# Performance work log

Hardware: AMD Instinct MI355X
Metric: run time of the kernel (lower is better)

The kernel has to match this reference:

```python
import jax, jax.numpy as jnp
import numpy as np

B, S, W = 128, 256, 1
DEPTH = 655            # MathTypeKeysMax
UNITS = 128
PROBLEM_BUCKETS = 32


def setup_inputs() -> dict:
    key = jax.random.key(0)
    ks = jax.random.split(key, 14)
    ri = lambda k, shape, hi: jax.random.randint(k, shape, 0, hi, dtype=jnp.int32)
    K = 4 * DEPTH * W  # flattened per-timestep feature width = 2620
    return {
        'move_count': ri(ks[0], (B,), 100),
        'moves_remaining': ri(ks[1], (B,), 100),
        'last_rule': ri(ks[2], (B,), 12),
        'node_count': ri(ks[3], (B,), 64),
        'problem_type': ri(ks[4], (B,), PROBLEM_BUCKETS),
        'bwd_vectors': ri(ks[5], (B, S, W), DEPTH),
        'fwd_vectors': ri(ks[6], (B, S, W), DEPTH),
        'last_bwd_vectors': ri(ks[7], (B, S, W), DEPTH),
        'last_fwd_vectors': ri(ks[8], (B, S, W), DEPTH),
        'W_dense': jax.random.normal(ks[9], (K, UNITS), jnp.float32) * (1.0 / np.sqrt(K)),
        'b_dense': jnp.zeros((UNITS,), jnp.float32),
        'Wx': jax.random.normal(ks[10], (UNITS, 4 * UNITS), jnp.float32) * (1.0 / np.sqrt(UNITS)),
        'Wh': jax.random.normal(ks[11], (UNITS, 4 * UNITS), jnp.float32) * (1.0 / np.sqrt(UNITS)),
        'b_lstm': jnp.zeros((4 * UNITS,), jnp.float32),
    }


def _lstm(x, Wx, Wh, b):
    # x: [B, S, U] -> (seq hidden [B, S, U], final hidden [B, U]); keras gate order i,f,c,o
    U = Wh.shape[0]
    bsz = x.shape[0]
    # precompute input projections once: [S, B, 4U]
    xz = jnp.einsum('bsu,uv->sbv', x, Wx) + b

    def step(carry, zt):
        h, c = carry
        z = zt + h @ Wh
        i, f, g, o = jnp.split(z, 4, axis=-1)
        i = jax.nn.sigmoid(i)
        f = jax.nn.sigmoid(f)
        g = jnp.tanh(g)
        o = jax.nn.sigmoid(o)
        c = f * c + i * g
        h = o * jnp.tanh(c)
        return (h, c), h

    init = (jnp.zeros((bsz, U), x.dtype), jnp.zeros((bsz, U), x.dtype))
    (h_last, _), hs = jax.lax.scan(step, init, xz)
    return jnp.transpose(hs, (1, 0, 2)), h_last


def reference(move_count, moves_remaining, last_rule, node_count, problem_type,
              bwd_vectors, fwd_vectors, last_bwd_vectors, last_fwd_vectors,
              W_dense, b_dense, Wx, Wh, b_lstm):
    f32 = lambda a: a.astype(jnp.float32)
    # DenseFeatures context extraction: 3 numeric int columns + 32-bucket indicator
    context_inputs = jnp.concatenate([
        f32(last_rule)[:, None],
        f32(move_count)[:, None],
        f32(node_count)[:, None],
        jax.nn.one_hot(problem_type, PROBLEM_BUCKETS, dtype=jnp.float32),
    ], axis=-1)  # [B, 35]

    sequence_length = bwd_vectors.shape[1]
    # one-hot each [B,S,W] sequence to [B,S,W,DEPTH], concat on last axis -> [B,S,W,4*DEPTH]
    oh = jnp.concatenate([
        jax.nn.one_hot(bwd_vectors, DEPTH, dtype=jnp.float32),
        jax.nn.one_hot(fwd_vectors, DEPTH, dtype=jnp.float32),
        jax.nn.one_hot(last_bwd_vectors, DEPTH, dtype=jnp.float32),
        jax.nn.one_hot(last_fwd_vectors, DEPTH, dtype=jnp.float32),
    ], axis=-1)
    bsz = oh.shape[0]
    # per-example Flatten keeps leading S dim, so the loop == one batched matmul
    flat = oh.reshape(bsz, sequence_length, -1)      # [B, S, 4*DEPTH*W]
    outputs = jnp.einsum('bsk,ku->bsu', flat, W_dense) + b_dense  # [B, S, U]

    hidden_states, lstm_vectors = _lstm(outputs, Wx, Wh, b_lstm)
    return (context_inputs, lstm_vectors, hidden_states, sequence_length)
```

## Files before the change

kernel.cpp:

```cpp
#include <hip/hip_runtime.h>
#include <cstdint>

#define BB   128
#define SS   256
#define NDEPTH 655
#define UU   128
#define VV   512
#define NPB  32

#define STEP_BARRIER()                                          \
    do {                                                        \
        asm volatile("s_waitcnt lgkmcnt(0)" ::: "memory");      \
        __builtin_amdgcn_s_barrier();                           \
        __builtin_amdgcn_sched_barrier(0);                      \
    } while (0)

__global__ void context_kernel(const int* __restrict__ last_rule,
                               const int* __restrict__ move_count,
                               const int* __restrict__ node_count,
                               const int* __restrict__ problem_type,
                               float* __restrict__ out, int write_seq) {
    int i = blockIdx.x * blockDim.x + threadIdx.x;
    if (i < BB * 35) {
        int b = i / 35, c = i % 35;
        float v;
        if (c == 0)      v = (float)last_rule[b];
        else if (c == 1) v = (float)move_count[b];
        else if (c == 2) v = (float)node_count[b];
        else             v = (problem_type[b] == (c - 3)) ? 1.0f : 0.0f;
        out[i] = v;
    }
    if (write_seq && i == 0)
        out[(size_t)BB*35 + (size_t)BB*UU + (size_t)BB*SS*UU] = (float)SS;
}

__global__ void wdwx_kernel(const float* __restrict__ Wd,
                            const float* __restrict__ Wx,
                            const float* __restrict__ b_dense,
                            const float* __restrict__ b_lstm,
                            float* __restrict__ WdWx,
                            float* __restrict__ base) {
    int v  = threadIdx.x;
    int k0 = blockIdx.x * 4;
    const float* wd0 = Wd + (size_t)k0 * UU;
    float a0 = 0.f, a1 = 0.f, a2 = 0.f, a3 = 0.f;
    for (int u = 0; u < UU; ++u) {
        float wx = Wx[u * VV + v];
        a0 = fmaf(wd0[u],        wx, a0);
        a1 = fmaf(wd0[UU + u],   wx, a1);
        a2 = fmaf(wd0[2*UU + u], wx, a2);
        a3 = fmaf(wd0[3*UU + u], wx, a3);
    }
    WdWx[(size_t)(k0+0)*VV + v] = a0;
    WdWx[(size_t)(k0+1)*VV + v] = a1;
    WdWx[(size_t)(k0+2)*VV + v] = a2;
    WdWx[(size_t)(k0+3)*VV + v] = a3;
    if (blockIdx.x == 0) {
        float a = 0.f;
        for (int u = 0; u < UU; ++u) a = fmaf(b_dense[u], Wx[u * VV + v], a);
        base[v] = a + b_lstm[v];
    }
}

__global__ __launch_bounds__(512, 2)
void lstm_kernel(const int* __restrict__ bwd,  const int* __restrict__ fwd,
                 const int* __restrict__ lbwd, const int* __restrict__ lfwd,
                 const float* __restrict__ WdWx,
                 const float* __restrict__ base,
                 const float* __restrict__ Wh,
                 float* __restrict__ hidden_states,
                 float* __restrict__ lstm_vectors) {
    const int b    = blockIdx.x;
    const int t    = threadIdx.x;
    const int lane = t & 63;
    const int w    = t >> 6;
    const int q    = lane & 3;
    const int u    = w * 16 + (lane >> 2);
    const int col  = q * UU + u;

    __shared__ __align__(16) float h_buf[2][144];
    __shared__ int idx_lds[SS][4];

    float wh[128];
    #pragma unroll
    for (int kk = 0; kk < 32; ++kk) {
        #pragma unroll
        for (int g = 0; g < 4; ++g)
            wh[kk*4+g] = Wh[(size_t)(32*q + kk) * VV + g*UU + u];
    }

    for (int s = t; s < SS; s += 512) {
        idx_lds[s][0] =            bwd [b*SS + s];
        idx_lds[s][1] =   NDEPTH + fwd [b*SS + s];
        idx_lds[s][2] = 2*NDEPTH + lbwd[b*SS + s];
        idx_lds[s][3] = 3*NDEPTH + lfwd[b*SS + s];
    }
    if (t < UU) h_buf[0][36*(t>>5) + (t&31)] = 0.0f;
    float c    = 0.0f;
    float bias = base[col];
    __syncthreads();

    float g0 = WdWx[(size_t)idx_lds[0][0] * VV + col];
    float g1 = WdWx[(size_t)idx_lds[0][1] * VV + col];
    float g2 = WdWx[(size_t)idx_lds[0][2] * VV + col];
    float g3 = WdWx[(size_t)idx_lds[0][3] * VV + col];

    const bool b0 = (q & 1) != 0;
    const bool b1 = (q & 2) != 0;

    int p = 0;
    for (int s = 0; s < SS; ++s) {
        float z = bias + (g0 + g1) + (g2 + g3);
        if (s + 1 < SS) {
            g0 = WdWx[(size_t)idx_lds[s+1][0] * VV + col];
            g1 = WdWx[(size_t)idx_lds[s+1][1] * VV + col];
            g2 = WdWx[(size_t)idx_lds[s+1][2] * VV + col];
            g3 = WdWx[(size_t)idx_lds[s+1][3] * VV + col];
        }

        const float* hb = h_buf[p] + 36 * q;
        float pp0 = 0.f, pp1 = 0.f, pp2 = 0.f, pp3 = 0.f;
        #pragma unroll
        for (int kk = 0; kk < 32; kk += 4) {
            float4 hv = *(const float4*)(hb + kk);
            pp0 = fmaf(hv.x, wh[(kk+0)*4+0], pp0);
            pp1 = fmaf(hv.x, wh[(kk+0)*4+1], pp1);
            pp2 = fmaf(hv.x, wh[(kk+0)*4+2], pp2);
            pp3 = fmaf(hv.x, wh[(kk+0)*4+3], pp3);
            pp0 = fmaf(hv.y, wh[(kk+1)*4+0], pp0);
            pp1 = fmaf(hv.y, wh[(kk+1)*4+1], pp1);
            pp2 = fmaf(hv.y, wh[(kk+1)*4+2], pp2);
            pp3 = fmaf(hv.y, wh[(kk+1)*4+3], pp3);
            pp0 = fmaf(hv.z, wh[(kk+2)*4+0], pp0);
            pp1 = fmaf(hv.z, wh[(kk+2)*4+1], pp1);
            pp2 = fmaf(hv.z, wh[(kk+2)*4+2], pp2);
            pp3 = fmaf(hv.z, wh[(kk+2)*4+3], pp3);
            pp0 = fmaf(hv.w, wh[(kk+3)*4+0], pp0);
            pp1 = fmaf(hv.w, wh[(kk+3)*4+1], pp1);
            pp2 = fmaf(hv.w, wh[(kk+3)*4+2], pp2);
            pp3 = fmaf(hv.w, wh[(kk+3)*4+3], pp3);
        }

        float keepA = b0 ? pp1 : pp0;
        float keepB = b0 ? pp3 : pp2;
        float sendA = b0 ? pp0 : pp1;
        float sendB = b0 ? pp2 : pp3;
        float sA = keepA + __shfl_xor(sendA, 1);
        float sB = keepB + __shfl_xor(sendB, 1);
        float send2 = b1 ? sA : sB;
        z += (b1 ? sB : sA) + __shfl_xor(send2, 2);

        float xs = (q == 2) ? 2.0f * z : z;
        float sg = __fdividef(1.0f, 1.0f + __expf(-xs));
        float a  = (q == 2) ? 2.0f * sg - 1.0f : sg;

        float v1 = __shfl_xor(a, 1);
        float v2 = __shfl_xor(a, 2);
        float v3 = __shfl_xor(v1, 2);
        float ig = (q & 1) ? v1 * v3 : a * v2;
        float gf = (q & 1) ? ((q & 2) ? v2 : a)
                           : ((q & 2) ? v3 : v1);
        float go = (q & 1) ? ((q & 2) ? a  : v2)
                           : ((q & 2) ? v1 : v3);
        c = fmaf(gf, c, ig);
        float e  = __expf(2.0f * c);
        float tc = 1.0f - __fdividef(2.0f, e + 1.0f);
        float h  = go * tc;

        if (q == 0) {
            h_buf[p ^ 1][36*(u>>5) + (u&31)] = h;
            hidden_states[((size_t)b * SS + s) * UU + u] = h;
        }
        STEP_BARRIER();
        p ^= 1;
    }
    if (t < UU) lstm_vectors[(size_t)b * UU + t] = h_buf[p][36*(t>>5) + (t&31)];
}

extern "C" void kernel_launch(void* const* d_in, const int* in_sizes, int n_in,
                              void* d_out, int out_size, void* d_ws, size_t ws_size,
                              hipStream_t stream) {
    const int* move_count   = (const int*)d_in[0];
    const int* last_rule    = (const int*)d_in[2];
    const int* node_count   = (const int*)d_in[3];
    const int* problem_type = (const int*)d_in[4];
    const int* bwd          = (const int*)d_in[5];
    const int* fwd          = (const int*)d_in[6];
    const int* lbwd         = (const int*)d_in[7];
    const int* lfwd         = (const int*)d_in[8];
    const float* Wd         = (const float*)d_in[9];
    const float* b_dense    = (const float*)d_in[10];
    const float* Wx         = (const float*)d_in[11];
    const float* Wh         = (const float*)d_in[12];
    const float* b_lstm     = (const float*)d_in[13];

    float* out  = (float*)d_out;
    float* WdWx = (float*)d_ws;
    float* base = WdWx + (size_t)(4 * NDEPTH) * VV;

    float* lstm_out = out + BB * 35;
    float* hs_out   = lstm_out + BB * UU;
    int write_seq = (out_size > BB*35 + BB*UU + BB*SS*UU) ? 1 : 0;

    context_kernel<<<(BB*35 + 255)/256, 256, 0, stream>>>(
        last_rule, move_count, node_count, problem_type, out, write_seq);
    wdwx_kernel<<<NDEPTH, VV, 0, stream>>>(Wd, Wx, b_dense, b_lstm, WdWx, base);
    lstm_kernel<<<BB, 512, 0, stream>>>(bwd, fwd, lbwd, lfwd, WdWx, base, Wh,
                                        hs_out, lstm_out);
}
```

Before: 316.9 us.

## Use fp16 dot2 for recurrent matvec, fuse context into WdWx kernel

The recurrent h·Wh product now keeps Wh and h in packed fp16 and uses the fdot2 instruction, halving LDS reads and FMA count per step on the serial critical path. The context kernel is folded into the WdWx precompute kernel, which now computes 20 rows per block over 131 blocks, removing one launch. The final hidden state is kept in a register instead of being reread from shared memory. Rounding h and Wh to fp16 adds error that accumulates over 256 recurrent steps.

```diff
diff --git a/kernel.cpp b/kernel.cpp
--- a/kernel.cpp
+++ b/kernel.cpp
@@ -7,6 +7,18 @@
 #define UU   128
 #define VV   512
 #define NPB  32
+#define ROWS_PER_BLK 20
+
+typedef _Float16 f16;
+typedef _Float16 f16x2 __attribute__((ext_vector_type(2)));
+
+#if __has_builtin(__builtin_amdgcn_fdot2)
+#define FDOT2(a, b, c) __builtin_amdgcn_fdot2((a), (b), (c), false)
+#else
+static __device__ __forceinline__ float FDOT2(f16x2 a, f16x2 b, float c) {
+    return c + (float)a.x * (float)b.x + (float)a.y * (float)b.y;
+}
+#endif
 
 #define STEP_BARRIER()                                          \
     do {                                                        \
@@ -15,49 +27,47 @@
         __builtin_amdgcn_sched_barrier(0);                      \
     } while (0)
 
-__global__ void context_kernel(const int* __restrict__ last_rule,
-                               const int* __restrict__ move_count,
-                               const int* __restrict__ node_count,
-                               const int* __restrict__ problem_type,
-                               float* __restrict__ out, int write_seq) {
-    int i = blockIdx.x * blockDim.x + threadIdx.x;
-    if (i < BB * 35) {
-        int b = i / 35, c = i % 35;
-        float v;
-        if (c == 0)      v = (float)last_rule[b];
-        else if (c == 1) v = (float)move_count[b];
-        else if (c == 2) v = (float)node_count[b];
-        else             v = (problem_type[b] == (c - 3)) ? 1.0f : 0.0f;
-        out[i] = v;
-    }
-    if (write_seq && i == 0)
-        out[(size_t)BB*35 + (size_t)BB*UU + (size_t)BB*SS*UU] = (float)SS;
-}
-
 __global__ void wdwx_kernel(const float* __restrict__ Wd,
                             const float* __restrict__ Wx,
                             const float* __restrict__ b_dense,
                             const float* __restrict__ b_lstm,
+                            const int* __restrict__ last_rule,
+                            const int* __restrict__ move_count,
+                            const int* __restrict__ node_count,
+                            const int* __restrict__ problem_type,
                             float* __restrict__ WdWx,
-                            float* __restrict__ base) {
-    int v  = threadIdx.x;
-    int k0 = blockIdx.x * 4;
-    const float* wd0 = Wd + (size_t)k0 * UU;
-    float a0 = 0.f, a1 = 0.f, a2 = 0.f, a3 = 0.f;
-    for (int u = 0; u < UU; ++u) {
-        float wx = Wx[u * VV + v];
-        a0 = fmaf(wd0[u],        wx, a0);
-        a1 = fmaf(wd0[UU + u],   wx, a1);
-        a2 = fmaf(wd0[2*UU + u], wx, a2);
-        a3 = fmaf(wd0[3*UU + u], wx, a3);
-    }
-    WdWx[(size_t)(k0+0)*VV + v] = a0;
-    WdWx[(size_t)(k0+1)*VV + v] = a1;
-    WdWx[(size_t)(k0+2)*VV + v] = a2;
-    WdWx[(size_t)(k0+3)*VV + v] = a3;
+                            float* __restrict__ base,
+                            float* __restrict__ out, int write_seq) {
+    const int v  = threadIdx.x;
+    const int k0 = blockIdx.x * ROWS_PER_BLK;
+
+    int gid = blockIdx.x * 512 + v;
+    if (gid < BB * 35) {
+        int b = gid / 35, cc = gid % 35;
+        float val;
+        if (cc == 0)      val = (float)last_rule[b];
+        else if (cc == 1) val = (float)move_count[b];
+        else if (cc == 2) val = (float)node_count[b];
+        else              val = (problem_type[b] == (cc - 3)) ? 1.0f : 0.0f;
+        out[gid] = val;
+    }
+    if (write_seq && gid == 0)
+        out[(size_t)BB*35 + (size_t)BB*UU + (size_t)BB*SS*UU] = (float)SS;
+
+    float acc[ROWS_PER_BLK] = {};
+    for (int uu = 0; uu < UU; ++uu) {
+        float wx = Wx[uu * VV + v];
+        #pragma unroll
+        for (int r = 0; r < ROWS_PER_BLK; ++r)
+            acc[r] = fmaf(Wd[(size_t)(k0 + r) * UU + uu], wx, acc[r]);
+    }
+    #pragma unroll
+    for (int r = 0; r < ROWS_PER_BLK; ++r)
+        WdWx[(size_t)(k0 + r) * VV + v] = acc[r];
+
     if (blockIdx.x == 0) {
         float a = 0.f;
-        for (int u = 0; u < UU; ++u) a = fmaf(b_dense[u], Wx[u * VV + v], a);
+        for (int uu = 0; uu < UU; ++uu) a = fmaf(b_dense[uu], Wx[uu * VV + v], a);
         base[v] = a + b_lstm[v];
     }
 }
@@ -78,15 +88,19 @@
     const int u    = w * 16 + (lane >> 2);
     const int col  = q * UU + u;
 
-    __shared__ __align__(16) float h_buf[2][144];
+    __shared__ __align__(16) unsigned char h2buf[2][320];
     __shared__ int idx_lds[SS][4];
 
-    float wh[128];
+    f16x2 wh2[64];
     #pragma unroll
-    for (int kk = 0; kk < 32; ++kk) {
+    for (int j = 0; j < 16; ++j) {
         #pragma unroll
-        for (int g = 0; g < 4; ++g)
-            wh[kk*4+g] = Wh[(size_t)(32*q + kk) * VV + g*UU + u];
+        for (int g = 0; g < 4; ++g) {
+            float w0 = Wh[(size_t)(32*q + 2*j    ) * VV + g*UU + u];
+            float w1 = Wh[(size_t)(32*q + 2*j + 1) * VV + g*UU + u];
+            f16x2 pk; pk.x = (f16)w0; pk.y = (f16)w1;
+            wh2[j*4 + g] = pk;
+        }
     }
 
     for (int s = t; s < SS; s += 512) {
@@ -95,9 +109,11 @@
         idx_lds[s][2] = 2*NDEPTH + lbwd[b*SS + s];
         idx_lds[s][3] = 3*NDEPTH + lfwd[b*SS + s];
     }
-    if (t < UU) h_buf[0][36*(t>>5) + (t&31)] = 0.0f;
-    float c    = 0.0f;
-    float bias = base[col];
+    if (t < UU)
+        ((f16*)(h2buf[0] + 80*(t >> 5)))[t & 31] = (f16)0.0f;
+    float c      = 0.0f;
+    float bias   = base[col];
+    float h_last = 0.0f;
     __syncthreads();
 
     float g0 = WdWx[(size_t)idx_lds[0][0] * VV + col];
@@ -118,28 +134,22 @@
             g3 = WdWx[(size_t)idx_lds[s+1][3] * VV + col];
         }
 
-        const float* hb = h_buf[p] + 36 * q;
+        const uint4* hb = (const uint4*)(h2buf[p] + 80 * q);
+        uint4 A = hb[0], Bv = hb[1], Cv = hb[2], Dv = hb[3];
         float pp0 = 0.f, pp1 = 0.f, pp2 = 0.f, pp3 = 0.f;
-        #pragma unroll
-        for (int kk = 0; kk < 32; kk += 4) {
-            float4 hv = *(const float4*)(hb + kk);
-            pp0 = fmaf(hv.x, wh[(kk+0)*4+0], pp0);
-            pp1 = fmaf(hv.x, wh[(kk+0)*4+1], pp1);
-            pp2 = fmaf(hv.x, wh[(kk+0)*4+2], pp2);
-            pp3 = fmaf(hv.x, wh[(kk+0)*4+3], pp3);
-            pp0 = fmaf(hv.y, wh[(kk+1)*4+0], pp0);
-            pp1 = fmaf(hv.y, wh[(kk+1)*4+1], pp1);
-            pp2 = fmaf(hv.y, wh[(kk+1)*4+2], pp2);
-            pp3 = fmaf(hv.y, wh[(kk+1)*4+3], pp3);
-            pp0 = fmaf(hv.z, wh[(kk+2)*4+0], pp0);
-            pp1 = fmaf(hv.z, wh[(kk+2)*4+1], pp1);
-            pp2 = fmaf(hv.z, wh[(kk+2)*4+2], pp2);
-            pp3 = fmaf(hv.z, wh[(kk+2)*4+3], pp3);
-            pp0 = fmaf(hv.w, wh[(kk+3)*4+0], pp0);
-            pp1 = fmaf(hv.w, wh[(kk+3)*4+1], pp1);
-            pp2 = fmaf(hv.w, wh[(kk+3)*4+2], pp2);
-            pp3 = fmaf(hv.w, wh[(kk+3)*4+3], pp3);
-        }
+        #define DOTW(word, j)                                            \
+            do {                                                         \
+                f16x2 hv = __builtin_bit_cast(f16x2, (word));            \
+                pp0 = FDOT2(hv, wh2[(j)*4+0], pp0);                      \
+                pp1 = FDOT2(hv, wh2[(j)*4+1], pp1);                      \
+                pp2 = FDOT2(hv, wh2[(j)*4+2], pp2);                      \
+                pp3 = FDOT2(hv, wh2[(j)*4+3], pp3);                      \
+            } while (0)
+        DOTW(A.x,  0); DOTW(A.y,  1); DOTW(A.z,  2); DOTW(A.w,  3);
+        DOTW(Bv.x, 4); DOTW(Bv.y, 5); DOTW(Bv.z, 6); DOTW(Bv.w, 7);
+        DOTW(Cv.x, 8); DOTW(Cv.y, 9); DOTW(Cv.z,10); DOTW(Cv.w,11);
+        DOTW(Dv.x,12); DOTW(Dv.y,13); DOTW(Dv.z,14); DOTW(Dv.w,15);
+        #undef DOTW
 
         float keepA = b0 ? pp1 : pp0;
         float keepB = b0 ? pp3 : pp2;
@@ -168,13 +178,14 @@
         float h  = go * tc;
 
         if (q == 0) {
-            h_buf[p ^ 1][36*(u>>5) + (u&31)] = h;
+            ((f16*)(h2buf[p ^ 1] + 80*(u >> 5)))[u & 31] = (f16)h;
             hidden_states[((size_t)b * SS + s) * UU + u] = h;
+            h_last = h;
         }
         STEP_BARRIER();
         p ^= 1;
     }
-    if (t < UU) lstm_vectors[(size_t)b * UU + t] = h_buf[p][36*(t>>5) + (t&31)];
+    if (q == 0) lstm_vectors[(size_t)b * UU + u] = h_last;
 }
 
 extern "C" void kernel_launch(void* const* d_in, const int* in_sizes, int n_in,
@@ -202,9 +213,9 @@
     float* hs_out   = lstm_out + BB * UU;
     int write_seq = (out_size > BB*35 + BB*UU + BB*SS*UU) ? 1 : 0;
 
-    context_kernel<<<(BB*35 + 255)/256, 256, 0, stream>>>(
-        last_rule, move_count, node_count, problem_type, out, write_seq);
-    wdwx_kernel<<<NDEPTH, VV, 0, stream>>>(Wd, Wx, b_dense, b_lstm, WdWx, base);
+    wdwx_kernel<<<131, VV, 0, stream>>>(Wd, Wx, b_dense, b_lstm,
+                                        last_rule, move_count, node_count,
+                                        problem_type, WdWx, base, out, write_seq);
     lstm_kernel<<<BB, 512, 0, stream>>>(bwd, fwd, lbwd, lfwd, WdWx, base, Wh,
                                         hs_out, lstm_out);
 }
```

Result: faster. 309.0 us (-2.5%).
